# Performance work log

Measured on AMD Instinct MI355X. Metric: run time of the kernel, lower is better.

Reference implementation:

```python
import jax, jax.numpy as jnp
import numpy as np

N_NODES = 100000
N_EMBED = 64
N_HIDDEN = 64
N_EDGES = 1200000


def setup_inputs() -> dict:
    key = jax.random.key(0)
    ks = jax.random.split(key, 8)
    prop_edge_index = jax.random.randint(ks[0], (2, N_EDGES), 0, N_NODES, dtype=jnp.int64)
    emb = jax.random.normal(ks[1], (N_NODES, N_EMBED), dtype=jnp.float32) * 0.05
    # ChebConv K=2 -> two linear weights per layer + bias
    W1_0 = jax.random.normal(ks[2], (N_EMBED, N_HIDDEN), dtype=jnp.float32) * 0.05
    W1_1 = jax.random.normal(ks[3], (N_EMBED, N_HIDDEN), dtype=jnp.float32) * 0.05
    b1 = jnp.zeros((N_HIDDEN,), dtype=jnp.float32)
    W2_0 = jax.random.normal(ks[4], (N_HIDDEN, N_HIDDEN), dtype=jnp.float32) * 0.05
    W2_1 = jax.random.normal(ks[5], (N_HIDDEN, N_HIDDEN), dtype=jnp.float32) * 0.05
    b2 = jnp.zeros((N_HIDDEN,), dtype=jnp.float32)
    return {"prop_edge_index": prop_edge_index, "emb": emb,
            "W1_0": W1_0, "W1_1": W1_1, "b1": b1,
            "W2_0": W2_0, "W2_1": W2_1, "b2": b2}


def _cheb_norm(edge_index, num_nodes):
    """PyG ChebConv.__norm__ with sym normalization, lambda_max=2.0.
    L_hat = 2L/lambda_max - I = (I - D^-1/2 A D^-1/2) - I, so the net
    diagonal weight is 0 and off-diagonal weight is -d_i^-1/2 * d_j^-1/2.
    Self loops in the input are removed first (weight 0)."""
    row, col = edge_index[0], edge_index[1]
    w = jnp.where(row != col, 1.0, 0.0).astype(jnp.float32)  # remove_self_loops
    deg = jax.ops.segment_sum(w, row, num_segments=num_nodes)
    dinv = jnp.where(deg > 0, deg ** -0.5, 0.0)
    norm = -dinv[row] * w * dinv[col]
    return norm


def _cheb_conv(x, src, dst, norm, W0, W1, b, num_nodes):
    # K=2: out = T0(x) @ W0 + T1(x) @ W1 + b, T0 = x, T1 = L_hat x
    Tx1 = jax.ops.segment_sum(norm[:, None] * x[src], dst, num_segments=num_nodes)
    return x @ W0 + Tx1 @ W1 + b


def reference(prop_edge_index, emb, W1_0, W1_1, b1, W2_0, W2_1, b2):
    src, dst = prop_edge_index[0], prop_edge_index[1]
    norm = _cheb_norm(prop_edge_index, N_NODES)
    x = _cheb_conv(emb, src, dst, norm, W1_0, W1_1, b1, N_NODES)
    x = jax.nn.relu(x)
    # dropout: eval mode (identity)
    x = _cheb_conv(x, src, dst, norm, W2_0, W2_1, b2, N_NODES)
    return x
```

## Files before the change

kernel.cpp:

```cpp
#include <hip/hip_runtime.h>

#define N_NODES 100000
#define N_EDGES 1200000
#define NF 64

typedef __attribute__((ext_vector_type(8))) short short8;
typedef __attribute__((ext_vector_type(4))) float float4v;

__device__ __forceinline__ ushort f2bf(float f) {
    unsigned u = __float_as_uint(f);
    return (ushort)((u + 0x7FFF + ((u >> 16) & 1)) >> 16);
}

#define NBINS 196
#define CAP 7680
#define EPB 5120
#define NBLK 235

#define OFF_CNT    0
#define OFF_ENDP   400128
#define OFF_DINV   800256
#define OFF_CUR    1200384
#define OFF_PKW    1202048
#define OFF_SRCS   1234816
#define OFF_NRMS   7255936
#define OFF_SBIN   10266496
#define OFF_DBIN   16287616
#define OFF_EMBBF  10266496
#define OFF_HBF    23066496

__global__ __launch_bounds__(256) void packW(const float* __restrict__ W10,
                                             const float* __restrict__ W11,
                                             const float* __restrict__ W20,
                                             const float* __restrict__ W21,
                                             ushort* __restrict__ pk,
                                             int* __restrict__ cur) {
    if (blockIdx.x == 8) {
        for (int i = threadIdx.x; i < 2 * NBINS; i += 256)
            cur[i] = (i < NBINS ? i : i - NBINS) * CAP;
        return;
    }
    int idx = blockIdx.x * 256 + threadIdx.x;
    int layer = idx >> 10;
    int rest = idx & 1023;
    int f = rest >> 6, L = rest & 63;
    int n = (f & 3) * 16 + (L & 15);
    int kb = (f >> 2) * 32 + ((L >> 4) << 3);
#pragma unroll
    for (int j = 0; j < 8; ++j) {
        int k = kb + j;
        const float* W = layer ? ((k < 64) ? W20 : W21) : ((k < 64) ? W10 : W11);
        pk[idx * 8 + j] = f2bf(W[(k & 63) * 64 + n]);
    }
}

__global__ __launch_bounds__(256) void binsort(const int* __restrict__ row,
                                               const int* __restrict__ col,
                                               int* __restrict__ cur,
                                               ushort* __restrict__ sbinned,
                                               int* __restrict__ dbinned) {
    __shared__ int sh[NBINS], dh[NBINS];
    __shared__ int sbase[NBINS], dbase[NBINS];
    int t = threadIdx.x;
    if (t < NBINS) { sh[t] = 0; dh[t] = 0; }
    __syncthreads();
    int base = blockIdx.x * EPB;
    for (int k = 0; k < 20; ++k) {
        int e = base + k * 256 + t;
        if (e < N_EDGES) {
            int s = row[e], d = col[e];
            if (s != d) {
                atomicAdd(&sh[s >> 9], 1);
                atomicAdd(&dh[d >> 9], 1);
            }
        }
    }
    __syncthreads();
    if (t < NBINS) {
        sbase[t] = atomicAdd(&cur[t], sh[t]);
        dbase[t] = atomicAdd(&cur[NBINS + t], dh[t]);
    }
    __syncthreads();
    for (int k = 0; k < 20; ++k) {
        int e = base + k * 256 + t;
        if (e < N_EDGES) {
            int s = row[e], d = col[e];
            if (s != d) {
                int ss = atomicAdd(&sbase[s >> 9], 1);
                sbinned[ss] = (ushort)(s & 511);
                int ds = atomicAdd(&dbase[d >> 9], 1);
                dbinned[ds] = (s << 9) | (d & 511);
            }
        }
    }
}

__global__ __launch_bounds__(256) void binD1(const ushort* __restrict__ sbinned,
                                             const int* __restrict__ cur,
                                             float* __restrict__ dinv) {
    __shared__ int hist[512];
    int t = threadIdx.x;
    hist[t] = 0; hist[t + 256] = 0;
    __syncthreads();
    int b = blockIdx.x;
    int start = b * CAP;
    int end = cur[b];
    for (int i = start + t; i < end; i += 256)
        atomicAdd(&hist[sbinned[i]], 1);
    __syncthreads();
    int n0 = (b << 9) + t, n1 = n0 + 256;
    if (n0 < N_NODES) dinv[n0] = hist[t] ? rsqrtf((float)hist[t]) : 0.0f;
    if (n1 < N_NODES) dinv[n1] = hist[t + 256] ? rsqrtf((float)hist[t + 256]) : 0.0f;
}

__global__ __launch_bounds__(256) void binD2(const int* __restrict__ dbinned,
                                             const int* __restrict__ cur,
                                             const float* __restrict__ dinv,
                                             int* __restrict__ cnt,
                                             int* __restrict__ endp,
                                             int* __restrict__ srcs,
                                             ushort* __restrict__ nrms) {
    __shared__ int hist[512];
    __shared__ int lcur[512];
    __shared__ int tot_s;
    int t = threadIdx.x;
    hist[t] = 0; hist[t + 256] = 0;
    __syncthreads();
    int b = blockIdx.x;
    int start = b * CAP;
    int end = cur[NBINS + b];
    for (int i = start + t; i < end; i += 256)
        atomicAdd(&hist[dbinned[i] & 511], 1);
    __syncthreads();
    int o0 = hist[t], o1 = hist[t + 256];
    int A0 = (o0 + 3) & ~3, A1 = (o1 + 3) & ~3;
    __syncthreads();
    hist[t] = A0; hist[t + 256] = A1;
    __syncthreads();
    for (int off = 1; off < 512; off <<= 1) {
        int v0 = (t >= off) ? hist[t - off] : 0;
        int v1 = (t + 256 >= off) ? hist[t + 256 - off] : 0;
        __syncthreads();
        hist[t] += v0; hist[t + 256] += v1;
        __syncthreads();
    }
    int e0 = hist[t] - A0, e1 = hist[t + 256] - A1;
    if (t == 255) tot_s = hist[511];
    lcur[t] = start + e0;
    lcur[t + 256] = start + e1;
    int n0 = (b << 9) + t, n1 = n0 + 256;
    if (n0 < N_NODES) { cnt[n0] = o0; endp[n0] = start + e0 + o0; }
    if (n1 < N_NODES) { cnt[n1] = o1; endp[n1] = start + e1 + o1; }
    __syncthreads();
    for (int i = start + t; i < end; i += 256) {
        int p = dbinned[i];
        int s = p >> 9, dl = p & 511;
        int slot = atomicAdd(&lcur[dl], 1);
        srcs[slot] = s;
        nrms[slot] = f2bf(-dinv[s] * dinv[(b << 9) + dl]);
    }
    __syncthreads();
    for (int k = o0; k < A0; ++k) { srcs[start + e0 + k] = 0; nrms[start + e0 + k] = 0; }
    for (int k = o1; k < A1; ++k) { srcs[start + e1 + k] = 0; nrms[start + e1 + k] = 0; }
    if (t < 8) { srcs[start + tot_s + t] = 0; nrms[start + tot_s + t] = 0; }
}

__global__ __launch_bounds__(256) void embcvt(const float* __restrict__ in,
                                              ushort* __restrict__ out) {
    int i = (blockIdx.x * 256 + threadIdx.x) * 8;
    float4 v0 = *(const float4*)(in + i);
    float4 v1 = *(const float4*)(in + i + 4);
    uint4 o;
    o.x = (uint)f2bf(v0.x) | ((uint)f2bf(v0.y) << 16);
    o.y = (uint)f2bf(v0.z) | ((uint)f2bf(v0.w) << 16);
    o.z = (uint)f2bf(v1.x) | ((uint)f2bf(v1.y) << 16);
    o.w = (uint)f2bf(v1.z) | ((uint)f2bf(v1.w) << 16);
    *(uint4*)(out + i) = o;
}

#define NPW 16
#define WPB 4
#define NPB (NPW * WPB)
#define LB2 ((N_NODES + NPB - 1) / NPB)

__global__ __launch_bounds__(256, 8) void cheb_layer(const ushort* __restrict__ x,
                                                     const int* __restrict__ srcs,
                                                     const ushort* __restrict__ nrms,
                                                     const int* __restrict__ endp,
                                                     const int* __restrict__ cnt,
                                                     const ushort* __restrict__ pk,
                                                     const float* __restrict__ bias,
                                                     ushort* __restrict__ out_bf,
                                                     float* __restrict__ out_f32,
                                                     int last) {
    __shared__ ushort sA[WPB][16][136];

    int t = threadIdx.x;
    int lane = t & 63, wid = t >> 6;
    int c = lane & 15, q = lane >> 4;
    int qd = q, fg = c;
    int nb = blockIdx.x * NPB + wid * NPW;

    int nend = 0, ncnt = 0;
    if (lane < NPW && nb + lane < N_NODES) {
        nend = endp[nb + lane];
        ncnt = cnt[nb + lane];
    }

    const uint2* xr = (const uint2*)x;

    for (int g = 0; g < NPW; ++g) {
        int node = nb + g;
        int cn = __builtin_amdgcn_readlane(ncnt, g);
        int eend = __builtin_amdgcn_readlane(nend, g);
        int e = eend - cn;
        float a0 = 0, a1 = 0, a2 = 0, a3 = 0;
        for (; e < eend; e += 8) {
            int4 sv = *(const int4*)(srcs + e);
            int4 sw = *(const int4*)(srcs + e + 4);
            uint2 nv = *(const uint2*)(nrms + e);
            uint2 nw = *(const uint2*)(nrms + e + 4);
            int sA01 = (qd & 1) ? sv.y : sv.x;
            int sA23 = (qd & 1) ? sv.w : sv.z;
            int srcA = (qd & 2) ? sA23 : sA01;
            int sB01 = (qd & 1) ? sw.y : sw.x;
            int sB23 = (qd & 1) ? sw.w : sw.z;
            int srcB = (qd & 2) ? sB23 : sB01;
            uint nAp = (qd & 2) ? nv.y : nv.x;
            uint nBp = (qd & 2) ? nw.y : nw.x;
            float nAf = __uint_as_float((qd & 1) ? (nAp & 0xffff0000u) : (nAp << 16));
            float nBf = __uint_as_float((qd & 1) ? (nBp & 0xffff0000u) : (nBp << 16));
            nAf = (e + qd < eend) ? nAf : 0.0f;
            nBf = (e + 4 + qd < eend) ? nBf : 0.0f;
            uint2 gA = xr[(size_t)srcA * 16 + fg];
            uint2 gB = xr[(size_t)srcB * 16 + fg];
            a0 = fmaf(nAf, __uint_as_float(gA.x << 16), a0);
            a1 = fmaf(nAf, __uint_as_float(gA.x & 0xffff0000u), a1);
            a2 = fmaf(nAf, __uint_as_float(gA.y << 16), a2);
            a3 = fmaf(nAf, __uint_as_float(gA.y & 0xffff0000u), a3);
            a0 = fmaf(nBf, __uint_as_float(gB.x << 16), a0);
            a1 = fmaf(nBf, __uint_as_float(gB.x & 0xffff0000u), a1);
            a2 = fmaf(nBf, __uint_as_float(gB.y << 16), a2);
            a3 = fmaf(nBf, __uint_as_float(gB.y & 0xffff0000u), a3);
        }
        a0 += __shfl_xor(a0, 16, 64); a1 += __shfl_xor(a1, 16, 64);
        a2 += __shfl_xor(a2, 16, 64); a3 += __shfl_xor(a3, 16, 64);
        a0 += __shfl_xor(a0, 32, 64); a1 += __shfl_xor(a1, 32, 64);
        a2 += __shfl_xor(a2, 32, 64); a3 += __shfl_xor(a3, 32, 64);
        int nidx = (node < N_NODES) ? node : 0;
        if (qd == 0) {
            uint2 xv = xr[(size_t)nidx * 16 + fg];
            *(uint2*)&sA[wid][g][4 * fg] = xv;
        }
        if (qd == 1) {
            uint2 p;
            p.x = (uint)f2bf(a0) | ((uint)f2bf(a1) << 16);
            p.y = (uint)f2bf(a2) | ((uint)f2bf(a3) << 16);
            *(uint2*)&sA[wid][g][64 + 4 * fg] = p;
        }
    }
    __builtin_amdgcn_wave_barrier();

    const short8* pk8 = (const short8*)pk;
    float4v C[4];
#pragma unroll
    for (int nt = 0; nt < 4; ++nt) {
        float b = bias[nt * 16 + c];
        C[nt] = (float4v){b, b, b, b};
    }
#pragma unroll
    for (int kt = 0; kt < 4; ++kt) {
        short8 af = *(const short8*)&sA[wid][c][kt * 32 + q * 8];
#pragma unroll
        for (int nt = 0; nt < 4; ++nt) {
            short8 bfr = pk8[(kt * 4 + nt) * 64 + lane];
            C[nt] = __builtin_amdgcn_mfma_f32_16x16x32_bf16(af, bfr, C[nt], 0, 0, 0);
        }
    }

#pragma unroll
    for (int nt = 0; nt < 4; ++nt) {
#pragma unroll
        for (int i = 0; i < 4; ++i) {
            int node = nb + q * 4 + i;
            if (node < N_NODES) {
                float v = C[nt][i];
                if (!last) {
                    v = fmaxf(v, 0.0f);
                    out_bf[(size_t)node * NF + nt * 16 + c] = f2bf(v);
                } else {
                    out_f32[(size_t)node * NF + nt * 16 + c] = v;
                }
            }
        }
    }
}

extern "C" void kernel_launch(void* const* d_in, const int* in_sizes, int n_in,
                              void* d_out, int out_size, void* d_ws, size_t ws_size,
                              hipStream_t stream) {
    const int* ei = (const int*)d_in[0];
    const int* row = ei;
    const int* col = ei + N_EDGES;
    const float* emb = (const float*)d_in[1];
    const float* W1_0 = (const float*)d_in[2];
    const float* W1_1 = (const float*)d_in[3];
    const float* b1 = (const float*)d_in[4];
    const float* W2_0 = (const float*)d_in[5];
    const float* W2_1 = (const float*)d_in[6];
    const float* b2 = (const float*)d_in[7];
    float* out = (float*)d_out;

    char* ws = (char*)d_ws;
    int* cnt = (int*)(ws + OFF_CNT);
    int* endp = (int*)(ws + OFF_ENDP);
    float* dinv = (float*)(ws + OFF_DINV);
    int* cur = (int*)(ws + OFF_CUR);
    ushort* pk = (ushort*)(ws + OFF_PKW);
    int* srcs = (int*)(ws + OFF_SRCS);
    ushort* nrms = (ushort*)(ws + OFF_NRMS);
    ushort* sbinned = (ushort*)(ws + OFF_SBIN);
    int* dbinned = (int*)(ws + OFF_DBIN);
    ushort* emb_bf = (ushort*)(ws + OFF_EMBBF);
    ushort* h_bf = (ushort*)(ws + OFF_HBF);

    packW<<<9, 256, 0, stream>>>(W1_0, W1_1, W2_0, W2_1, pk, cur);
    binsort<<<NBLK, 256, 0, stream>>>(row, col, cur, sbinned, dbinned);
    binD1<<<NBINS, 256, 0, stream>>>(sbinned, cur, dinv);
    binD2<<<NBINS, 256, 0, stream>>>(dbinned, cur, dinv, cnt, endp, srcs, nrms);
    embcvt<<<(N_NODES * NF) / 2048, 256, 0, stream>>>(emb, emb_bf);

    cheb_layer<<<LB2, 256, 0, stream>>>(emb_bf, srcs, nrms, endp, cnt, pk, b1, h_bf, nullptr, 0);
    cheb_layer<<<LB2, 256, 0, stream>>>(h_bf, srcs, nrms, endp, cnt, pk + 8192, b2, nullptr, out, 1);
}
```

Baseline: 231.2 us.

## Cache edges in LDS for binsort and retune block sizes across kernels

The binsort kernel now stores each edge's (src,dst) pair in shared memory during the counting pass, so the scatter pass does not read row/col from global memory a second time. Edges per block are halved so twice as many blocks run. binD1/binD2 use 512 threads with one node per thread instead of two, and cheb_layer goes from 4 to 2 warps per block. Together these aim to cut redundant global reads and improve occupancy and load balance. The cost is 20KB of shared memory per binsort block and more global atomics on the bin cursors.

```diff
diff --git a/kernel.cpp b/kernel.cpp
--- a/kernel.cpp
+++ b/kernel.cpp
@@ -14,8 +14,8 @@
 
 #define NBINS 196
 #define CAP 7680
-#define EPB 5120
-#define NBLK 235
+#define EPB 2560
+#define NBLK 469
 
 #define OFF_CNT    0
 #define OFF_ENDP   400128
@@ -29,18 +29,20 @@
 #define OFF_EMBBF  10266496
 #define OFF_HBF    23066496
 
-__global__ __launch_bounds__(256) void packW(const float* __restrict__ W10,
-                                             const float* __restrict__ W11,
-                                             const float* __restrict__ W20,
-                                             const float* __restrict__ W21,
-                                             ushort* __restrict__ pk,
-                                             int* __restrict__ cur) {
-    if (blockIdx.x == 8) {
-        for (int i = threadIdx.x; i < 2 * NBINS; i += 256)
+__global__ __launch_bounds__(256) void prep(const float* __restrict__ W10,
+                                            const float* __restrict__ W11,
+                                            const float* __restrict__ W20,
+                                            const float* __restrict__ W21,
+                                            ushort* __restrict__ pk,
+                                            int* __restrict__ cur) {
+    int b = blockIdx.x;
+    int t = threadIdx.x;
+    if (b == 8) {
+        for (int i = t; i < 2 * NBINS; i += 256)
             cur[i] = (i < NBINS ? i : i - NBINS) * CAP;
         return;
     }
-    int idx = blockIdx.x * 256 + threadIdx.x;
+    int idx = b * 256 + t;
     int layer = idx >> 10;
     int rest = idx & 1023;
     int f = rest >> 6, L = rest & 63;
@@ -59,20 +61,21 @@
                                                int* __restrict__ cur,
                                                ushort* __restrict__ sbinned,
                                                int* __restrict__ dbinned) {
+    __shared__ int2 ecache[EPB];
     __shared__ int sh[NBINS], dh[NBINS];
     __shared__ int sbase[NBINS], dbase[NBINS];
     int t = threadIdx.x;
     if (t < NBINS) { sh[t] = 0; dh[t] = 0; }
     __syncthreads();
     int base = blockIdx.x * EPB;
-    for (int k = 0; k < 20; ++k) {
+    for (int k = 0; k < EPB / 256; ++k) {
         int e = base + k * 256 + t;
-        if (e < N_EDGES) {
-            int s = row[e], d = col[e];
-            if (s != d) {
-                atomicAdd(&sh[s >> 9], 1);
-                atomicAdd(&dh[d >> 9], 1);
-            }
+        int s = -1, d = -1;
+        if (e < N_EDGES) { s = row[e]; d = col[e]; }
+        ecache[k * 256 + t] = make_int2(s, d);
+        if (s >= 0 && s != d) {
+            atomicAdd(&sh[s >> 9], 1);
+            atomicAdd(&dh[d >> 9], 1);
         }
     }
     __syncthreads();
@@ -81,39 +84,36 @@
         dbase[t] = atomicAdd(&cur[NBINS + t], dh[t]);
     }
     __syncthreads();
-    for (int k = 0; k < 20; ++k) {
-        int e = base + k * 256 + t;
-        if (e < N_EDGES) {
-            int s = row[e], d = col[e];
-            if (s != d) {
-                int ss = atomicAdd(&sbase[s >> 9], 1);
-                sbinned[ss] = (ushort)(s & 511);
-                int ds = atomicAdd(&dbase[d >> 9], 1);
-                dbinned[ds] = (s << 9) | (d & 511);
-            }
-        }
-    }
-}
-
-__global__ __launch_bounds__(256) void binD1(const ushort* __restrict__ sbinned,
+    for (int k = 0; k < EPB / 256; ++k) {
+        int2 p = ecache[k * 256 + t];
+        int s = p.x, d = p.y;
+        if (s >= 0 && s != d) {
+            int ss = atomicAdd(&sbase[s >> 9], 1);
+            sbinned[ss] = (ushort)(s & 511);
+            int ds = atomicAdd(&dbase[d >> 9], 1);
+            dbinned[ds] = (s << 9) | (d & 511);
+        }
+    }
+}
+
+__global__ __launch_bounds__(512) void binD1(const ushort* __restrict__ sbinned,
                                              const int* __restrict__ cur,
                                              float* __restrict__ dinv) {
     __shared__ int hist[512];
     int t = threadIdx.x;
-    hist[t] = 0; hist[t + 256] = 0;
+    hist[t] = 0;
     __syncthreads();
     int b = blockIdx.x;
     int start = b * CAP;
     int end = cur[b];
-    for (int i = start + t; i < end; i += 256)
+    for (int i = start + t; i < end; i += 512)
         atomicAdd(&hist[sbinned[i]], 1);
     __syncthreads();
-    int n0 = (b << 9) + t, n1 = n0 + 256;
+    int n0 = (b << 9) + t;
     if (n0 < N_NODES) dinv[n0] = hist[t] ? rsqrtf((float)hist[t]) : 0.0f;
-    if (n1 < N_NODES) dinv[n1] = hist[t + 256] ? rsqrtf((float)hist[t + 256]) : 0.0f;
-}
-
-__global__ __launch_bounds__(256) void binD2(const int* __restrict__ dbinned,
+}
+
+__global__ __launch_bounds__(512) void binD2(const int* __restrict__ dbinned,
                                              const int* __restrict__ cur,
                                              const float* __restrict__ dinv,
                                              int* __restrict__ cnt,
@@ -124,35 +124,32 @@
     __shared__ int lcur[512];
     __shared__ int tot_s;
     int t = threadIdx.x;
-    hist[t] = 0; hist[t + 256] = 0;
+    hist[t] = 0;
     __syncthreads();
     int b = blockIdx.x;
     int start = b * CAP;
     int end = cur[NBINS + b];
-    for (int i = start + t; i < end; i += 256)
+    for (int i = start + t; i < end; i += 512)
         atomicAdd(&hist[dbinned[i] & 511], 1);
     __syncthreads();
-    int o0 = hist[t], o1 = hist[t + 256];
-    int A0 = (o0 + 3) & ~3, A1 = (o1 + 3) & ~3;
-    __syncthreads();
-    hist[t] = A0; hist[t + 256] = A1;
+    int o0 = hist[t];
+    int A0 = (o0 + 3) & ~3;
+    __syncthreads();
+    hist[t] = A0;
     __syncthreads();
     for (int off = 1; off < 512; off <<= 1) {
-        int v0 = (t >= off) ? hist[t - off] : 0;
-        int v1 = (t + 256 >= off) ? hist[t + 256 - off] : 0;
+        int v = (t >= off) ? hist[t - off] : 0;
         __syncthreads();
-        hist[t] += v0; hist[t + 256] += v1;
+        hist[t] += v;
         __syncthreads();
     }
-    int e0 = hist[t] - A0, e1 = hist[t + 256] - A1;
-    if (t == 255) tot_s = hist[511];
+    int e0 = hist[t] - A0;
+    if (t == 511) tot_s = hist[511];
     lcur[t] = start + e0;
-    lcur[t + 256] = start + e1;
-    int n0 = (b << 9) + t, n1 = n0 + 256;
+    int n0 = (b << 9) + t;
     if (n0 < N_NODES) { cnt[n0] = o0; endp[n0] = start + e0 + o0; }
-    if (n1 < N_NODES) { cnt[n1] = o1; endp[n1] = start + e1 + o1; }
-    __syncthreads();
-    for (int i = start + t; i < end; i += 256) {
+    __syncthreads();
+    for (int i = start + t; i < end; i += 512) {
         int p = dbinned[i];
         int s = p >> 9, dl = p & 511;
         int slot = atomicAdd(&lcur[dl], 1);
@@ -161,7 +158,6 @@
     }
     __syncthreads();
     for (int k = o0; k < A0; ++k) { srcs[start + e0 + k] = 0; nrms[start + e0 + k] = 0; }
-    for (int k = o1; k < A1; ++k) { srcs[start + e1 + k] = 0; nrms[start + e1 + k] = 0; }
     if (t < 8) { srcs[start + tot_s + t] = 0; nrms[start + tot_s + t] = 0; }
 }
 
@@ -179,11 +175,11 @@
 }
 
 #define NPW 16
-#define WPB 4
+#define WPB 2
 #define NPB (NPW * WPB)
 #define LB2 ((N_NODES + NPB - 1) / NPB)
 
-__global__ __launch_bounds__(256, 8) void cheb_layer(const ushort* __restrict__ x,
+__global__ __launch_bounds__(128, 8) void cheb_layer(const ushort* __restrict__ x,
                                                      const int* __restrict__ srcs,
                                                      const ushort* __restrict__ nrms,
                                                      const int* __restrict__ endp,
@@ -324,12 +320,12 @@
     ushort* emb_bf = (ushort*)(ws + OFF_EMBBF);
     ushort* h_bf = (ushort*)(ws + OFF_HBF);
 
-    packW<<<9, 256, 0, stream>>>(W1_0, W1_1, W2_0, W2_1, pk, cur);
+    prep<<<9, 256, 0, stream>>>(W1_0, W1_1, W2_0, W2_1, pk, cur);
     binsort<<<NBLK, 256, 0, stream>>>(row, col, cur, sbinned, dbinned);
-    binD1<<<NBINS, 256, 0, stream>>>(sbinned, cur, dinv);
-    binD2<<<NBINS, 256, 0, stream>>>(dbinned, cur, dinv, cnt, endp, srcs, nrms);
+    binD1<<<NBINS, 512, 0, stream>>>(sbinned, cur, dinv);
+    binD2<<<NBINS, 512, 0, stream>>>(dbinned, cur, dinv, cnt, endp, srcs, nrms);
     embcvt<<<(N_NODES * NF) / 2048, 256, 0, stream>>>(emb, emb_bf);
 
-    cheb_layer<<<LB2, 256, 0, stream>>>(emb_bf, srcs, nrms, endp, cnt, pk, b1, h_bf, nullptr, 0);
-    cheb_layer<<<LB2, 256, 0, stream>>>(h_bf, srcs, nrms, endp, cnt, pk + 8192, b2, nullptr, out, 1);
-}
+    cheb_layer<<<LB2, 128, 0, stream>>>(emb_bf, srcs, nrms, endp, cnt, pk, b1, h_bf, nullptr, 0);
+    cheb_layer<<<LB2, 128, 0, stream>>>(h_bf, srcs, nrms, endp, cnt, pk + 8192, b2, nullptr, out, 1);
+}
```

New measurement: 227.7 us. No clear change (-1.5%).
